# Performance work log

Hardware: AMD Instinct MI355X
Metric: run time of the kernel (lower is better)

The kernel has to match this reference:

```python
import jax, jax.numpy as jnp
import numpy as np

HEADS = 16  # init kwarg heads

def setup_inputs() -> dict:
    key = jax.random.key(0)
    kx, kq, kk, kv = jax.random.split(key, 4)
    B, C, H, W = 8, 256, 128, 128
    c_out = 256
    s = 1.0 / np.sqrt(C)
    return {
        "x": jax.random.normal(kx, (B, C, H, W), dtype=jnp.float32),
        "wq": jax.random.normal(kq, (c_out, C), dtype=jnp.float32) * s,
        "wk": jax.random.normal(kk, (c_out, C), dtype=jnp.float32) * s,
        "wv": jax.random.normal(kv, (c_out, C), dtype=jnp.float32) * s,
    }

def _feature_map(t):
    return jax.nn.elu(t) + 1.0

def reference(x, wq, wk, wv):
    B, C, H, W = x.shape
    M = H * W
    c_out = wq.shape[0]
    dh = c_out // HEADS
    # 1x1 conv (no bias) == channel matmul; reshape to [B, heads, dh, M]
    def proj(w):
        return jnp.einsum('bchw,oc->bohw', x, w).reshape(B, HEADS, dh, M)
    q = _feature_map(proj(wq))
    k = _feature_map(proj(wk))
    v = proj(wv)
    # original: kv = einsum('bhdk,bhdm->bhkm', k, v); out = einsum('bhdk,bhkm->bhdm', q, kv)
    # reassociated (identical math, avoids [M,M] intermediate):
    A = jnp.einsum('bhdm,bhem->bhde', q, k)          # [B,h,dh,dh]
    out = jnp.einsum('bhde,bhem->bhdm', A, v)         # [B,h,dh,M]
    # z = 1/(einsum('bhdk,bhdm->bhm', q, k.sum(-1, keepdims=True)) + 1e-6) -> [B,h,1]
    z = 1.0 / (jnp.einsum('bhdm,bhd->bh', q, k.sum(-1)) + 1e-6)
    # torch: out * z.unsqueeze(1) with z [B,h,1] -> [B,1,h,1]; requires dh == heads
    out = out * z[:, None, :, None]
    return out.reshape(B, HEADS * dh, H, W)
```

## Files before the change

kernel.cpp:

```cpp
#include <hip/hip_runtime.h>

typedef unsigned short ushortT;
typedef unsigned int uintT;
typedef __attribute__((ext_vector_type(8))) short s8v;
typedef __attribute__((ext_vector_type(4))) float f4v;

#define MFMA16(a,b,c) __builtin_amdgcn_mfma_f32_16x16x32_bf16(a,b,c,0,0,0)
#define MTOT 16384
#define XT_STRIDE 264
#define XT_BATCH (16384 * 264)
#define XBUF_SH 16896
#define XBUF_B  33792

#define GLL(g, l, sz) __builtin_amdgcn_global_load_lds( \
    (const __attribute__((address_space(1))) void*)(g), \
    (__attribute__((address_space(3))) void*)(l), (sz), 0, 0)

__device__ __forceinline__ ushortT f2bf(float f) {
    uintT u = __float_as_uint(f);
    u += 0x7FFFu + ((u >> 16) & 1u);
    return (ushortT)(u >> 16);
}
__device__ __forceinline__ uintT pack2(float a, float b) {
    return (uintT)f2bf(a) | ((uintT)f2bf(b) << 16);
}
__device__ __forceinline__ float elu1(float p) {
    return p > 0.f ? p + 1.f : __expf(p);
}

__global__ void k_prep(const float* __restrict__ wq, const float* __restrict__ wk,
                       ushortT* __restrict__ wqk, float* __restrict__ accz)
{
    int i = blockIdx.x * 256 + threadIdx.x;
    wqk[i]         = f2bf(wq[i]);
    wqk[65536 + i] = f2bf(wk[i]);
    if (i < 36864) accz[i] = 0.f;
}

__global__ __launch_bounds__(256) void k_tx(const float* __restrict__ x,
                                            ushortT* __restrict__ xt)
{
    __shared__ ushortT tile[64 * 68];
    const int t = threadIdx.x;
    const int m0 = blockIdx.x * 64;
    const int ct = blockIdx.y & 3, b = blockIdx.y >> 2;
    const int c0 = ct * 64;

    const int cl = t >> 4, ml = (t & 15) * 4;
    #pragma unroll
    for (int i = 0; i < 4; ++i) {
        f4v v = *(const f4v*)(x + ((size_t)(b * 256 + c0 + cl + i * 16)) * MTOT + m0 + ml);
        uintT* w = (uintT*)&tile[(cl + i * 16) * 68 + ml];
        w[0] = pack2(v.x, v.y);
        w[1] = pack2(v.z, v.w);
    }
    __syncthreads();
    const int mr = t >> 2, cc = (t & 3) * 16;
    s8v o0, o1;
    #pragma unroll
    for (int u = 0; u < 8; ++u) o0[u] = (short)tile[(cc + u) * 68 + mr];
    #pragma unroll
    for (int u = 0; u < 8; ++u) o1[u] = (short)tile[(cc + 8 + u) * 68 + mr];
    ushortT* dst = xt + (size_t)b * XT_BATCH + (size_t)(m0 + mr) * XT_STRIDE + c0 + cc;
    *(s8v*)dst = o0;
    *(s8v*)(dst + 8) = o1;
}

__global__ __launch_bounds__(256, 2) void k_qk(
    const ushortT* __restrict__ xt, const ushortT* __restrict__ wqk,
    float* __restrict__ Ag, float* __restrict__ qsg, float* __restrict__ ksg)
{
    __shared__ __align__(16) ushortT lds[2 * XBUF_SH + 4 * 1280];
    const int t = threadIdx.x;
    const int wv = t >> 6, lane = t & 63, quad = lane >> 4, l15 = lane & 15;
    const int b = blockIdx.y;
    const size_t xtb = (size_t)b * XT_BATCH + (size_t)(blockIdx.x * 256) * XT_STRIDE;

    ushortT* gram = lds + 2 * XBUF_SH + wv * 1280;
    float* gramf = (float*)gram;

    f4v accA[4];
    float qacc[4][4], kacc[4][4];
    #pragma unroll
    for (int i = 0; i < 4; ++i) {
        accA[i] = (f4v){0,0,0,0};
        #pragma unroll
        for (int r = 0; r < 4; ++r) { qacc[i][r] = 0.f; kacc[i][r] = 0.f; }
    }

    const ushortT* wq_base = wqk + (wv * 64 + l15) * 256 + quad * 8;
    const ushortT* wk_base = wq_base + 65536;

    {
        const char* gb = (const char*)(xt + xtb);
        char* lb = (char*)lds;
        #pragma unroll
        for (int i = 0; i < 8; ++i) GLL(gb + i * 4096 + t * 16, lb + i * 4096 + t * 16, 16);
        GLL(gb + 32768 + t * 4, lb + 32768 + t * 4, 4);
    }

    for (int tt = 0; tt < 4; ++tt) {
        __syncthreads();
        if (tt < 3) {
            const char* gb = (const char*)(xt + xtb) + (size_t)(tt + 1) * (64 * XT_STRIDE * 2);
            char* lb = (char*)lds + ((tt + 1) & 1) * XBUF_B;
            #pragma unroll
            for (int i = 0; i < 8; ++i) GLL(gb + i * 4096 + t * 16, lb + i * 4096 + t * 16, 16);
            GLL(gb + 32768 + t * 4, lb + 32768 + t * 4, 4);
        }
        const ushortT* xb = lds + (tt & 1) * XBUF_SH;

        f4v aq[4][4], ak[4][4];
        #pragma unroll
        for (int i = 0; i < 4; ++i)
            #pragma unroll
            for (int j = 0; j < 4; ++j) { aq[i][j] = (f4v){0,0,0,0}; ak[i][j] = (f4v){0,0,0,0}; }

        #pragma unroll 2
        for (int kc = 0; kc < 8; ++kc) {
            s8v afq[4], afk[4], bf[4];
            #pragma unroll
            for (int ot = 0; ot < 4; ++ot)
                afq[ot] = *(const s8v*)(wq_base + ot * 16 * 256 + kc * 32);
            #pragma unroll
            for (int ot = 0; ot < 4; ++ot)
                afk[ot] = *(const s8v*)(wk_base + ot * 16 * 256 + kc * 32);
            #pragma unroll
            for (int j = 0; j < 4; ++j)
                bf[j] = *(const s8v*)&xb[(j * 16 + l15) * XT_STRIDE + kc * 32 + quad * 8];
            #pragma unroll
            for (int ot = 0; ot < 4; ++ot)
                #pragma unroll
                for (int j = 0; j < 4; ++j)
                    aq[ot][j] = MFMA16(afq[ot], bf[j], aq[ot][j]);
            #pragma unroll
            for (int ot = 0; ot < 4; ++ot)
                #pragma unroll
                for (int j = 0; j < 4; ++j)
                    ak[ot][j] = MFMA16(afk[ot], bf[j], ak[ot][j]);
        }

        #pragma unroll
        for (int ot = 0; ot < 4; ++ot)
            #pragma unroll
            for (int j = 0; j < 4; ++j)
                #pragma unroll
                for (int r = 0; r < 4; ++r) {
                    aq[ot][j][r] = elu1(aq[ot][j][r]);
                    ak[ot][j][r] = elu1(ak[ot][j][r]);
                }

        #pragma unroll
        for (int ot = 0; ot < 4; ++ot)
            #pragma unroll
            for (int r = 0; r < 4; ++r) {
                float sq = aq[ot][0][r] + aq[ot][1][r] + aq[ot][2][r] + aq[ot][3][r];
                float sk = ak[ot][0][r] + ak[ot][1][r] + ak[ot][2][r] + ak[ot][3][r];
                #pragma unroll
                for (int off = 1; off < 16; off <<= 1) {
                    sq += __shfl_xor(sq, off);
                    sk += __shfl_xor(sk, off);
                }
                qacc[ot][r] += sq;
                kacc[ot][r] += sk;
            }

        #pragma unroll
        for (int hf = 0; hf < 2; ++hf)
            #pragma unroll
            for (int ot = 0; ot < 4; ++ot) {
                #pragma unroll
                for (int jj = 0; jj < 2; ++jj)
                    #pragma unroll
                    for (int r = 0; r < 4; ++r) {
                        int d = quad * 4 + r;
                        gram[d * 40 + jj * 16 + l15]        = f2bf(aq[ot][hf * 2 + jj][r]);
                        gram[(16 + d) * 40 + jj * 16 + l15] = f2bf(ak[ot][hf * 2 + jj][r]);
                    }
                s8v qa = *(const s8v*)&gram[l15 * 40 + quad * 8];
                s8v kb = *(const s8v*)&gram[(16 + l15) * 40 + quad * 8];
                accA[ot] = MFMA16(qa, kb, accA[ot]);
            }
    }

    #pragma unroll
    for (int ot = 0; ot < 4; ++ot)
        #pragma unroll
        for (int r = 0; r < 4; ++r)
            atomicAdd(Ag + ((b * 16 + wv * 4 + ot) * 16 + quad * 4 + r) * 16 + l15, accA[ot][r]);

    if (l15 == 0) {
        #pragma unroll
        for (int ot = 0; ot < 4; ++ot)
            #pragma unroll
            for (int r = 0; r < 4; ++r) {
                int row = ot * 16 + quad * 4 + r;
                gramf[row]      = qacc[ot][r];
                gramf[64 + row] = kacc[ot][r];
            }
    }
    float myq = gramf[lane];
    float myk = gramf[64 + lane];
    atomicAdd(qsg + b * 256 + wv * 64 + lane, myq);
    atomicAdd(ksg + b * 256 + wv * 64 + lane, myk);
}

__global__ __launch_bounds__(256) void k_weff(
    const float* __restrict__ wvw, const float* __restrict__ Ag,
    const float* __restrict__ qsg, const float* __restrict__ ksg,
    ushortT* __restrict__ weff)
{
    __shared__ float A_l[256];
    __shared__ float z_l[16];
    const int t = threadIdx.x;
    const int h = blockIdx.x, b = blockIdx.y;
    A_l[t] = Ag[(b * 16 + h) * 256 + t];
    if (t < 16) {
        float s = 0.f;
        #pragma unroll
        for (int d = 0; d < 16; ++d)
            s += qsg[b * 256 + t * 16 + d] * ksg[b * 256 + t * 16 + d];
        z_l[t] = 1.f / (s + 1e-6f);
    }
    __syncthreads();
    float acc[16];
    #pragma unroll
    for (int d = 0; d < 16; ++d) acc[d] = 0.f;
    #pragma unroll 4
    for (int e = 0; e < 16; ++e) {
        float w = wvw[(h * 16 + e) * 256 + t];
        #pragma unroll
        for (int d = 0; d < 16; ++d) acc[d] += A_l[d * 16 + e] * w;
    }
    #pragma unroll
    for (int d = 0; d < 16; ++d)
        weff[((size_t)b * 256 + h * 16 + d) * 256 + t] = f2bf(acc[d] * z_l[d]);
}

__global__ __launch_bounds__(256, 2) void k_out(
    const ushortT* __restrict__ xt, const ushortT* __restrict__ weff,
    float* __restrict__ out)
{
    __shared__ __align__(16) ushortT lds[2 * XBUF_SH];
    const int t = threadIdx.x;
    const int wv = t >> 6, lane = t & 63, quad = lane >> 4, l15 = lane & 15;
    const int b = blockIdx.y;
    const size_t xtb = (size_t)b * XT_BATCH + (size_t)(blockIdx.x * 256) * XT_STRIDE;

    const ushortT* w_base = weff + (size_t)b * 65536 + (wv * 64 + l15) * 256 + quad * 8;

    {
        const char* gb = (const char*)(xt + xtb);
        char* lb = (char*)lds;
        #pragma unroll
        for (int i = 0; i < 8; ++i) GLL(gb + i * 4096 + t * 16, lb + i * 4096 + t * 16, 16);
        GLL(gb + 32768 + t * 4, lb + 32768 + t * 4, 4);
    }

    for (int tt = 0; tt < 4; ++tt) {
        __syncthreads();
        if (tt < 3) {
            const char* gb = (const char*)(xt + xtb) + (size_t)(tt + 1) * (64 * XT_STRIDE * 2);
            char* lb = (char*)lds + ((tt + 1) & 1) * XBUF_B;
            #pragma unroll
            for (int i = 0; i < 8; ++i) GLL(gb + i * 4096 + t * 16, lb + i * 4096 + t * 16, 16);
            GLL(gb + 32768 + t * 4, lb + 32768 + t * 4, 4);
        }
        const ushortT* xb = lds + (tt & 1) * XBUF_SH;

        f4v acc[4][4];
        #pragma unroll
        for (int i = 0; i < 4; ++i)
            #pragma unroll
            for (int j = 0; j < 4; ++j) acc[i][j] = (f4v){0,0,0,0};

        #pragma unroll 2
        for (int kc = 0; kc < 8; ++kc) {
            s8v af[4], bf[4];
            #pragma unroll
            for (int ot = 0; ot < 4; ++ot)
                af[ot] = *(const s8v*)(w_base + ot * 16 * 256 + kc * 32);
            #pragma unroll
            for (int j = 0; j < 4; ++j)
                bf[j] = *(const s8v*)&xb[(j * 16 + l15) * XT_STRIDE + kc * 32 + quad * 8];
            #pragma unroll
            for (int ot = 0; ot < 4; ++ot)
                #pragma unroll
                for (int j = 0; j < 4; ++j)
                    acc[ot][j] = MFMA16(af[ot], bf[j], acc[ot][j]);
        }

        const int m0 = (blockIdx.x * 4 + tt) * 64;
        #pragma unroll
        for (int ot = 0; ot < 4; ++ot)
            #pragma unroll
            for (int j = 0; j < 4; ++j)
                #pragma unroll
                for (int r = 0; r < 4; ++r)
                    out[((size_t)b * 256 + wv * 64 + ot * 16 + quad * 4 + r) * MTOT
                        + m0 + j * 16 + l15] = acc[ot][j][r];
    }
}

extern "C" void kernel_launch(void* const* d_in, const int* in_sizes, int n_in,
                              void* d_out, int out_size, void* d_ws, size_t ws_size,
                              hipStream_t stream)
{
    const float* x   = (const float*)d_in[0];
    const float* wq  = (const float*)d_in[1];
    const float* wk  = (const float*)d_in[2];
    const float* wvw = (const float*)d_in[3];
    float* out = (float*)d_out;
    char* ws = (char*)d_ws;
    ushortT* wqk  = (ushortT*)ws;
    float*   Ag   = (float*)(ws + 262144);
    float*   qsg  = (float*)(ws + 393216);
    float*   ksg  = (float*)(ws + 401408);
    ushortT* weff = (ushortT*)(ws + 409600);
    ushortT* xt   = (ushortT*)(ws + 1458176);

    hipLaunchKernelGGL(k_prep, dim3(256), dim3(256), 0, stream, wq, wk, wqk, Ag);
    hipLaunchKernelGGL(k_tx,   dim3(256, 32), dim3(256), 0, stream, x, xt);
    hipLaunchKernelGGL(k_qk,   dim3(64, 8), dim3(256), 0, stream, xt, wqk, Ag, qsg, ksg);
    hipLaunchKernelGGL(k_weff, dim3(16, 8),  dim3(256), 0, stream, wvw, Ag, qsg, ksg, weff);
    hipLaunchKernelGGL(k_out,  dim3(64, 8), dim3(256), 0, stream, xt, weff, out);
}
```

Before: 387.5 us.

## Halve x-tile to 32 positions, compute q/k sums via MFMA with ones

The k_qk and k_out kernels now stage 32 spatial positions per step instead of 64, running eight pipeline steps instead of four. This halves LDS use per block and shrinks the accumulator register footprint, with the aim of raising occupancy. In k_qk, the per-row sums of q and k were computed with shuffle reductions. They are now computed by extra MFMAs against a vector of bf16 ones, reusing the fragments already loaded for the Gram matrix. The k_tx transpose tile padding also changes from 68 to 66. The trade-off is more barriers and weight-fragment reloads per position, plus sums that are now taken from bf16-rounded values.

```diff
diff --git a/kernel.cpp b/kernel.cpp
--- a/kernel.cpp
+++ b/kernel.cpp
@@ -9,12 +9,20 @@
 #define MTOT 16384
 #define XT_STRIDE 264
 #define XT_BATCH (16384 * 264)
-#define XBUF_SH 16896
-#define XBUF_B  33792
+#define XB32_SH 8448
+#define XB32_B  16896
 
 #define GLL(g, l, sz) __builtin_amdgcn_global_load_lds( \
     (const __attribute__((address_space(1))) void*)(g), \
     (__attribute__((address_space(3))) void*)(l), (sz), 0, 0)
+
+#define STAGE32(tt2) do { \
+    const char* gb_ = (const char*)(xt + xtb) + (size_t)(tt2) * XB32_B; \
+    char* lb_ = (char*)lds + (((tt2) & 1) ? XB32_B : 0); \
+    _Pragma("unroll") \
+    for (int i_ = 0; i_ < 4; ++i_) GLL(gb_ + i_ * 4096 + t * 16, lb_ + i_ * 4096 + t * 16, 16); \
+    if (t < 128) GLL(gb_ + 16384 + t * 4, lb_ + 16384 + t * 4, 4); \
+} while (0)
 
 __device__ __forceinline__ ushortT f2bf(float f) {
     uintT u = __float_as_uint(f);
@@ -40,7 +48,7 @@
 __global__ __launch_bounds__(256) void k_tx(const float* __restrict__ x,
                                             ushortT* __restrict__ xt)
 {
-    __shared__ ushortT tile[64 * 68];
+    __shared__ ushortT tile[64 * 66];
     const int t = threadIdx.x;
     const int m0 = blockIdx.x * 64;
     const int ct = blockIdx.y & 3, b = blockIdx.y >> 2;
@@ -50,7 +58,7 @@
     #pragma unroll
     for (int i = 0; i < 4; ++i) {
         f4v v = *(const f4v*)(x + ((size_t)(b * 256 + c0 + cl + i * 16)) * MTOT + m0 + ml);
-        uintT* w = (uintT*)&tile[(cl + i * 16) * 68 + ml];
+        uintT* w = (uintT*)&tile[(cl + i * 16) * 66 + ml];
         w[0] = pack2(v.x, v.y);
         w[1] = pack2(v.z, v.w);
     }
@@ -58,9 +66,9 @@
     const int mr = t >> 2, cc = (t & 3) * 16;
     s8v o0, o1;
     #pragma unroll
-    for (int u = 0; u < 8; ++u) o0[u] = (short)tile[(cc + u) * 68 + mr];
-    #pragma unroll
-    for (int u = 0; u < 8; ++u) o1[u] = (short)tile[(cc + 8 + u) * 68 + mr];
+    for (int u = 0; u < 8; ++u) o0[u] = (short)tile[(cc + u) * 66 + mr];
+    #pragma unroll
+    for (int u = 0; u < 8; ++u) o1[u] = (short)tile[(cc + 8 + u) * 66 + mr];
     ushortT* dst = xt + (size_t)b * XT_BATCH + (size_t)(m0 + mr) * XT_STRIDE + c0 + cc;
     *(s8v*)dst = o0;
     *(s8v*)(dst + 8) = o1;
@@ -70,55 +78,45 @@
     const ushortT* __restrict__ xt, const ushortT* __restrict__ wqk,
     float* __restrict__ Ag, float* __restrict__ qsg, float* __restrict__ ksg)
 {
-    __shared__ __align__(16) ushortT lds[2 * XBUF_SH + 4 * 1280];
+    __shared__ __align__(16) ushortT lds[2 * XB32_SH + 4 * 1280];
     const int t = threadIdx.x;
     const int wv = t >> 6, lane = t & 63, quad = lane >> 4, l15 = lane & 15;
     const int b = blockIdx.y;
     const size_t xtb = (size_t)b * XT_BATCH + (size_t)(blockIdx.x * 256) * XT_STRIDE;
 
-    ushortT* gram = lds + 2 * XBUF_SH + wv * 1280;
+    ushortT* gram = lds + 2 * XB32_SH + wv * 1280;
     float* gramf = (float*)gram;
 
-    f4v accA[4];
-    float qacc[4][4], kacc[4][4];
+    f4v accA[4], sQ[4], sK[4];
     #pragma unroll
     for (int i = 0; i < 4; ++i) {
         accA[i] = (f4v){0,0,0,0};
-        #pragma unroll
-        for (int r = 0; r < 4; ++r) { qacc[i][r] = 0.f; kacc[i][r] = 0.f; }
-    }
+        sQ[i]   = (f4v){0,0,0,0};
+        sK[i]   = (f4v){0,0,0,0};
+    }
+    s8v ones;
+    #pragma unroll
+    for (int u = 0; u < 8; ++u) ones[u] = (short)0x3F80;
 
     const ushortT* wq_base = wqk + (wv * 64 + l15) * 256 + quad * 8;
     const ushortT* wk_base = wq_base + 65536;
 
-    {
-        const char* gb = (const char*)(xt + xtb);
-        char* lb = (char*)lds;
-        #pragma unroll
-        for (int i = 0; i < 8; ++i) GLL(gb + i * 4096 + t * 16, lb + i * 4096 + t * 16, 16);
-        GLL(gb + 32768 + t * 4, lb + 32768 + t * 4, 4);
-    }
-
-    for (int tt = 0; tt < 4; ++tt) {
+    STAGE32(0);
+
+    for (int tt = 0; tt < 8; ++tt) {
         __syncthreads();
-        if (tt < 3) {
-            const char* gb = (const char*)(xt + xtb) + (size_t)(tt + 1) * (64 * XT_STRIDE * 2);
-            char* lb = (char*)lds + ((tt + 1) & 1) * XBUF_B;
-            #pragma unroll
-            for (int i = 0; i < 8; ++i) GLL(gb + i * 4096 + t * 16, lb + i * 4096 + t * 16, 16);
-            GLL(gb + 32768 + t * 4, lb + 32768 + t * 4, 4);
-        }
-        const ushortT* xb = lds + (tt & 1) * XBUF_SH;
-
-        f4v aq[4][4], ak[4][4];
+        if (tt < 7) STAGE32(tt + 1);
+        const ushortT* xb = lds + (tt & 1) * XB32_SH;
+
+        f4v aq[4][2], ak[4][2];
         #pragma unroll
         for (int i = 0; i < 4; ++i)
             #pragma unroll
-            for (int j = 0; j < 4; ++j) { aq[i][j] = (f4v){0,0,0,0}; ak[i][j] = (f4v){0,0,0,0}; }
+            for (int j = 0; j < 2; ++j) { aq[i][j] = (f4v){0,0,0,0}; ak[i][j] = (f4v){0,0,0,0}; }
 
         #pragma unroll 2
         for (int kc = 0; kc < 8; ++kc) {
-            s8v afq[4], afk[4], bf[4];
+            s8v afq[4], afk[4], bf[2];
             #pragma unroll
             for (int ot = 0; ot < 4; ++ot)
                 afq[ot] = *(const s8v*)(wq_base + ot * 16 * 256 + kc * 32);
@@ -126,24 +124,24 @@
             for (int ot = 0; ot < 4; ++ot)
                 afk[ot] = *(const s8v*)(wk_base + ot * 16 * 256 + kc * 32);
             #pragma unroll
-            for (int j = 0; j < 4; ++j)
+            for (int j = 0; j < 2; ++j)
                 bf[j] = *(const s8v*)&xb[(j * 16 + l15) * XT_STRIDE + kc * 32 + quad * 8];
             #pragma unroll
             for (int ot = 0; ot < 4; ++ot)
                 #pragma unroll
-                for (int j = 0; j < 4; ++j)
+                for (int j = 0; j < 2; ++j)
                     aq[ot][j] = MFMA16(afq[ot], bf[j], aq[ot][j]);
             #pragma unroll
             for (int ot = 0; ot < 4; ++ot)
                 #pragma unroll
-                for (int j = 0; j < 4; ++j)
+                for (int j = 0; j < 2; ++j)
                     ak[ot][j] = MFMA16(afk[ot], bf[j], ak[ot][j]);
         }
 
         #pragma unroll
         for (int ot = 0; ot < 4; ++ot)
             #pragma unroll
-            for (int j = 0; j < 4; ++j)
+            for (int j = 0; j < 2; ++j)
                 #pragma unroll
                 for (int r = 0; r < 4; ++r) {
                     aq[ot][j][r] = elu1(aq[ot][j][r]);
@@ -151,36 +149,21 @@
                 }
 
         #pragma unroll
-        for (int ot = 0; ot < 4; ++ot)
-            #pragma unroll
-            for (int r = 0; r < 4; ++r) {
-                float sq = aq[ot][0][r] + aq[ot][1][r] + aq[ot][2][r] + aq[ot][3][r];
-                float sk = ak[ot][0][r] + ak[ot][1][r] + ak[ot][2][r] + ak[ot][3][r];
-                #pragma unroll
-                for (int off = 1; off < 16; off <<= 1) {
-                    sq += __shfl_xor(sq, off);
-                    sk += __shfl_xor(sk, off);
+        for (int ot = 0; ot < 4; ++ot) {
+            #pragma unroll
+            for (int jj = 0; jj < 2; ++jj)
+                #pragma unroll
+                for (int r = 0; r < 4; ++r) {
+                    int d = quad * 4 + r;
+                    gram[d * 40 + jj * 16 + l15]        = f2bf(aq[ot][jj][r]);
+                    gram[(16 + d) * 40 + jj * 16 + l15] = f2bf(ak[ot][jj][r]);
                 }
-                qacc[ot][r] += sq;
-                kacc[ot][r] += sk;
-            }
-
-        #pragma unroll
-        for (int hf = 0; hf < 2; ++hf)
-            #pragma unroll
-            for (int ot = 0; ot < 4; ++ot) {
-                #pragma unroll
-                for (int jj = 0; jj < 2; ++jj)
-                    #pragma unroll
-                    for (int r = 0; r < 4; ++r) {
-                        int d = quad * 4 + r;
-                        gram[d * 40 + jj * 16 + l15]        = f2bf(aq[ot][hf * 2 + jj][r]);
-                        gram[(16 + d) * 40 + jj * 16 + l15] = f2bf(ak[ot][hf * 2 + jj][r]);
-                    }
-                s8v qa = *(const s8v*)&gram[l15 * 40 + quad * 8];
-                s8v kb = *(const s8v*)&gram[(16 + l15) * 40 + quad * 8];
-                accA[ot] = MFMA16(qa, kb, accA[ot]);
-            }
+            s8v qa = *(const s8v*)&gram[l15 * 40 + quad * 8];
+            s8v kb = *(const s8v*)&gram[(16 + l15) * 40 + quad * 8];
+            accA[ot] = MFMA16(qa, kb, accA[ot]);
+            sQ[ot]   = MFMA16(qa, ones, sQ[ot]);
+            sK[ot]   = MFMA16(kb, ones, sK[ot]);
+        }
     }
 
     #pragma unroll
@@ -195,8 +178,8 @@
             #pragma unroll
             for (int r = 0; r < 4; ++r) {
                 int row = ot * 16 + quad * 4 + r;
-                gramf[row]      = qacc[ot][r];
-                gramf[64 + row] = kacc[ot][r];
+                gramf[row]      = sQ[ot][r];
+                gramf[64 + row] = sK[ot][r];
             }
     }
     float myq = gramf[lane];
@@ -241,7 +224,7 @@
     const ushortT* __restrict__ xt, const ushortT* __restrict__ weff,
     float* __restrict__ out)
 {
-    __shared__ __align__(16) ushortT lds[2 * XBUF_SH];
+    __shared__ __align__(16) ushortT lds[2 * XB32_SH];
     const int t = threadIdx.x;
     const int wv = t >> 6, lane = t & 63, quad = lane >> 4, l15 = lane & 15;
     const int b = blockIdx.y;
@@ -249,52 +232,40 @@
 
     const ushortT* w_base = weff + (size_t)b * 65536 + (wv * 64 + l15) * 256 + quad * 8;
 
-    {
-        const char* gb = (const char*)(xt + xtb);
-        char* lb = (char*)lds;
-        #pragma unroll
-        for (int i = 0; i < 8; ++i) GLL(gb + i * 4096 + t * 16, lb + i * 4096 + t * 16, 16);
-        GLL(gb + 32768 + t * 4, lb + 32768 + t * 4, 4);
-    }
-
-    for (int tt = 0; tt < 4; ++tt) {
+    STAGE32(0);
+
+    for (int tt = 0; tt < 8; ++tt) {
         __syncthreads();
-        if (tt < 3) {
-            const char* gb = (const char*)(xt + xtb) + (size_t)(tt + 1) * (64 * XT_STRIDE * 2);
-            char* lb = (char*)lds + ((tt + 1) & 1) * XBUF_B;
-            #pragma unroll
-            for (int i = 0; i < 8; ++i) GLL(gb + i * 4096 + t * 16, lb + i * 4096 + t * 16, 16);
-            GLL(gb + 32768 + t * 4, lb + 32768 + t * 4, 4);
-        }
-        const ushortT* xb = lds + (tt & 1) * XBUF_SH;
-
-        f4v acc[4][4];
+        if (tt < 7) STAGE32(tt + 1);
+        const ushortT* xb = lds + (tt & 1) * XB32_SH;
+
+        f4v acc[4][2];
         #pragma unroll
         for (int i = 0; i < 4; ++i)
             #pragma unroll
-            for (int j = 0; j < 4; ++j) acc[i][j] = (f4v){0,0,0,0};
+            for (int j = 0; j < 2; ++j) acc[i][j] = (f4v){0,0,0,0};
 
         #pragma unroll 2
         for (int kc = 0; kc < 8; ++kc) {
-            s8v af[4], bf[4];
+            s8v af[4], bf[2];
             #pragma unroll
             for (int ot = 0; ot < 4; ++ot)
                 af[ot] = *(const s8v*)(w_base + ot * 16 * 256 + kc * 32);
             #pragma unroll
-            for (int j = 0; j < 4; ++j)
+            for (int j = 0; j < 2; ++j)
                 bf[j] = *(const s8v*)&xb[(j * 16 + l15) * XT_STRIDE + kc * 32 + quad * 8];
             #pragma unroll
             for (int ot = 0; ot < 4; ++ot)
                 #pragma unroll
-                for (int j = 0; j < 4; ++j)
+                for (int j = 0; j < 2; ++j)
                     acc[ot][j] = MFMA16(af[ot], bf[j], acc[ot][j]);
         }
 
-        const int m0 = (blockIdx.x * 4 + tt) * 64;
+        const int m0 = blockIdx.x * 256 + tt * 32;
         #pragma unroll
         for (int ot = 0; ot < 4; ++ot)
             #pragma unroll
-            for (int j = 0; j < 4; ++j)
+            for (int j = 0; j < 2; ++j)
                 #pragma unroll
                 for (int r = 0; r < 4; ++r)
                     out[((size_t)b * 256 + wv * 64 + ot * 16 + quad * 4 + r) * MTOT
```

New measurement: 448.5 us. 15.7% more time.
